# Optimization experiments

Hardware: AMD Instinct MI355X
Metric: run time of the kernel (lower is better)

The kernel has to match this reference:

```python
import jax, jax.numpy as jnp
import numpy as np

# Hardcoded class-anchor table from the original module's target_map ('0'..'9').
_TARGET_MAP = np.array([
    [0, 0.333, 0.333, 0.333, 0.333, 0.333, 0.333, 0.333, 0.333, 0.333],
    [1, 0.0, 0.0, 0.0, 0.0, 0.0, 0.0, 0.0, 0.0, 0.0],
    [0, -0.118, 0.943, -0.118, -0.118, -0.118, -0.118, -0.118, -0.118, -0.118],
    [0, -0.134, 1.78e-16, 0.935, -0.134, -0.134, -0.134, -0.134, -0.134, -0.134],
    [0, -0.154, 1.999e-16, 3.997e-16, 0.926, -0.154, -0.154, -0.154, -0.154, -0.154],
    [0, -0.183, 1.824e-16, 3.953e-16, 6.081e-17, 0.913, -0.183, -0.183, -0.183, -0.183],
    [0, -0.224, 1.738e-16, 4.469e-16, 7.448e-17, -9.93e-17, 0.894, -0.224, -0.224, -0.224],
    [0, -0.289, 2.134e-16, 4.914e-16, 6.41e-17, -1.282e-16, 1.282e-16, 0.866, -0.289, -0.289],
    [0, -0.408, 3.108e-16, 7.576e-16, 9.712e-17, -1.165e-16, 2.331e-16, -3.885e-17, 0.816, -0.408],
    [0, -0.707, 5.103e-16, 1.178e-15, 1.963e-16, -1.57e-16, 3.14e-16, -3.925e-17, -2.355e-16, 0.707],
], dtype=np.float32)

MARGIN_ADV_ANCHOR = 0.5
MARGIN_ADV_MOST_CONFUSING = 0.5
BATCH = 4_000_000
NUM_CLASSES = 10


def setup_inputs() -> dict:
    key = jax.random.key(0)
    k1, k2 = jax.random.split(key)
    x1 = jax.random.normal(k1, (BATCH, NUM_CLASSES), dtype=jnp.float32)
    target = jax.random.randint(k2, (BATCH,), 0, NUM_CLASSES, dtype=jnp.int64 if jax.config.jax_enable_x64 else jnp.int32)
    emb = jnp.asarray(_TARGET_MAP)  # [10, 10] constant class-anchor table
    return {"x1": x1, "target": target, "emb": emb}


def reference(x1, target, emb):
    # Gather per-sample anchor embedding (replaces the per-element python loop).
    x2 = emb[target]                              # [B, 10]
    x1_norm = jnp.sqrt(jnp.sum(x1 * x1, axis=1))  # [B]
    x2_norm = jnp.sqrt(jnp.sum(x2 * x2, axis=1))  # [B]
    adv_anchor_cos = 1.0 - jnp.sum(x1 * x2, axis=1) / (x1_norm * x2_norm)

    # Normalize x1, score against every class anchor in one GEMM.
    x1n = x1 / x1_norm[:, None]                   # [B, 10]
    score = jnp.einsum('bd,cd->bc', x1n, emb)     # [B, 10]

    # Most-confusing class: best-scoring class, or second-best if it equals the label.
    _, top2 = jax.lax.top_k(score, 2)             # [B, 2] int indices
    mc = jnp.where(top2[:, 0] != target, top2[:, 0], top2[:, 1])  # [B]

    x2b = emb[mc]                                 # [B, 10]
    x1n_norm = jnp.sqrt(jnp.sum(x1n * x1n, axis=1))
    x2b_norm = jnp.sqrt(jnp.sum(x2b * x2b, axis=1))
    adv_mc_cos = 1.0 - jnp.sum(x1n * x2b, axis=1) / (x1n_norm * x2b_norm)

    penalty_loss = jnp.maximum(MARGIN_ADV_MOST_CONFUSING - adv_mc_cos, 0.0)
    anchor_loss = jnp.maximum(adv_anchor_cos - MARGIN_ADV_ANCHOR, 0.0)
    return jnp.mean(penalty_loss + anchor_loss)
```

## Files before the change

### kernel.cpp

```cpp
#include <hip/hip_runtime.h>

#define NC 10
#define SPC 512
#define F4PC ((SPC * NC) / 4)
#define NBLOCKS 2048

typedef float f32x4 __attribute__((ext_vector_type(4)));

__device__ __forceinline__ float sample_loss(const float* x, int tg, const float* icn)
{
    float T8 = x[9];
    float T7 = x[8] + T8;
    float T6 = x[7] + T7;
    float T5 = x[6] + T6;
    float T4 = x[5] + T5;
    float T3 = x[4] + T4;
    float T2 = x[3] + T3;
    float T1 = x[2] + T2;
    float S  = x[1] + T1;

    float d[NC];
    d[0] = 0.333f * S;
    d[1] = x[0];
    d[2] = fmaf(0.943f, x[2], -0.118f * (x[1] + T2));
    d[3] = fmaf(0.935f, x[3], -0.134f * (x[1] + T3));
    d[4] = fmaf(0.926f, x[4], -0.154f * (x[1] + T4));
    d[5] = fmaf(0.913f, x[5], -0.183f * (x[1] + T5));
    d[6] = fmaf(0.894f, x[6], -0.224f * (x[1] + T6));
    d[7] = fmaf(0.866f, x[7], -0.289f * (x[1] + T7));
    d[8] = fmaf(0.816f, x[8], -0.408f * (x[1] + T8));
    d[9] = 0.707f * (x[9] - x[1]);

    float self = x[0] * x[0];
#pragma unroll
    for (int i = 1; i < NC; ++i) self = fmaf(x[i], x[i], self);
    float inv1 = __frsqrt_rn(self);

    float best = -3.0e38f, icnb = 1.f, dt = 0.f, icnt = 1.f;
#pragma unroll
    for (int c = 0; c < NC; ++c) {
        bool istg = (c == tg);
        dt   = istg ? d[c]   : dt;
        icnt = istg ? icn[c] : icnt;
        float dc = istg ? -3.0e38f : d[c];
        bool gt = dc > best;
        best = gt ? dc     : best;
        icnb = gt ? icn[c] : icnb;
    }
    float simmc = best * icnb * inv1;
    float simt  = dt   * icnt * inv1;
    return fmaxf(simmc - 0.5f, 0.f) + fmaxf(0.5f - simt, 0.f);
}

__global__ __launch_bounds__(256) void margin_loss_kernel(
    const float* __restrict__ x1,
    const int* __restrict__ target,
    float* __restrict__ partial,
    int B)
{
    __shared__ float lds[SPC * NC];
    __shared__ float swave[4];

    constexpr float N2[NC] = {
        9.f * 0.333f * 0.333f,
        1.f,
        0.943f * 0.943f + 8.f * 0.118f * 0.118f,
        0.935f * 0.935f + 7.f * 0.134f * 0.134f,
        0.926f * 0.926f + 6.f * 0.154f * 0.154f,
        0.913f * 0.913f + 5.f * 0.183f * 0.183f,
        0.894f * 0.894f + 4.f * 0.224f * 0.224f,
        0.866f * 0.866f + 3.f * 0.289f * 0.289f,
        0.816f * 0.816f + 2.f * 0.408f * 0.408f,
        2.f * 0.707f * 0.707f
    };
    float icn[NC];
#pragma unroll
    for (int c = 0; c < NC; ++c) icn[c] = __frsqrt_rn(N2[c]);

    const int tid = threadIdx.x;
    const f32x4* __restrict__ x14 = (const f32x4*)x1;
    f32x4* lds4 = (f32x4*)lds;
    const long maxf4 = (long)B * NC / 4;
    const int nchunks = (B + SPC - 1) / SPC;
    float local = 0.f;

    for (int chunk = blockIdx.x; chunk < nchunks; chunk += (int)gridDim.x) {
        long base = (long)chunk * F4PC;
        if (base + F4PC <= maxf4) {
#pragma unroll
            for (int k = 0; k < 5; ++k)
                lds4[k * 256 + tid] = __builtin_nontemporal_load(&x14[base + k * 256 + tid]);
        } else {
#pragma unroll
            for (int k = 0; k < 5; ++k) {
                long g = base + k * 256 + tid;
                if (g > maxf4 - 1) g = maxf4 - 1;
                lds4[k * 256 + tid] = __builtin_nontemporal_load(&x14[g]);
            }
        }
        __syncthreads();

        int s0 = chunk * SPC + tid * 2;
        const f32x4* vf = (const f32x4*)(lds + tid * 20);
        if (s0 + 1 < B) {
            long long tt = __builtin_nontemporal_load((const long long*)(target + s0));
            int tga = (int)(tt & 0xffffffff);
            int tgb = (int)(tt >> 32);
            f32x4 a0 = vf[0], a1 = vf[1], a2 = vf[2], a3 = vf[3], a4 = vf[4];
            float xa[NC] = {a0.x,a0.y,a0.z,a0.w,a1.x,a1.y,a1.z,a1.w,a2.x,a2.y};
            float xb[NC] = {a2.z,a2.w,a3.x,a3.y,a3.z,a3.w,a4.x,a4.y,a4.z,a4.w};
            local += sample_loss(xa, tga, icn);
            local += sample_loss(xb, tgb, icn);
        } else if (s0 < B) {
            f32x4 a0 = vf[0], a1 = vf[1], a2 = vf[2];
            float xa[NC] = {a0.x,a0.y,a0.z,a0.w,a1.x,a1.y,a1.z,a1.w,a2.x,a2.y};
            local += sample_loss(xa, target[s0], icn);
        }
        __syncthreads();
    }

#pragma unroll
    for (int off = 32; off > 0; off >>= 1) local += __shfl_down(local, off, 64);
    int lane = tid & 63;
    int wid  = tid >> 6;
    if (lane == 0) swave[wid] = local;
    __syncthreads();
    if (tid == 0)
        partial[blockIdx.x] = swave[0] + swave[1] + swave[2] + swave[3];
}

__global__ __launch_bounds__(256) void reduce_kernel(
    const float* __restrict__ partial, float* __restrict__ out, int n, float scale)
{
    float local = 0.f;
    for (int i = threadIdx.x; i < n; i += 256) local += partial[i];
#pragma unroll
    for (int off = 32; off > 0; off >>= 1) local += __shfl_down(local, off, 64);
    __shared__ float swave[4];
    int lane = threadIdx.x & 63;
    int wid  = threadIdx.x >> 6;
    if (lane == 0) swave[wid] = local;
    __syncthreads();
    if (threadIdx.x == 0)
        out[0] = (swave[0] + swave[1] + swave[2] + swave[3]) * scale;
}

extern "C" void kernel_launch(void* const* d_in, const int* in_sizes, int n_in,
                              void* d_out, int out_size, void* d_ws, size_t ws_size,
                              hipStream_t stream) {
    const float* x1     = (const float*)d_in[0];
    const int*   target = (const int*)d_in[1];
    float* out     = (float*)d_out;
    float* partial = (float*)d_ws;
    int B = in_sizes[1];

    margin_loss_kernel<<<NBLOCKS, 256, 0, stream>>>(x1, target, partial, B);
    reduce_kernel<<<1, 256, 0, stream>>>(partial, out, NBLOCKS, 1.0f / (float)B);
}
```

Baseline: 221.3 us.

## Replace LDS-staged chunk loop with register double-buffered direct per-thread loads

Removes the shared-memory staging and the two block barriers per chunk. Each thread now loads its two samples' 80 bytes and targets directly into registers in a grid-stride loop, prefetching the next pair while computing the current one. This is meant to keep more memory requests in flight and avoid barrier stalls. The cost is strided, less coalesced per-instruction access patterns and higher register pressure. An odd trailing sample is handled separately by one thread.

```diff
diff --git a/kernel.cpp b/kernel.cpp
--- a/kernel.cpp
+++ b/kernel.cpp
@@ -1,11 +1,29 @@
 #include <hip/hip_runtime.h>
 
 #define NC 10
-#define SPC 512
-#define F4PC ((SPC * NC) / 4)
 #define NBLOCKS 2048
+#define NTHREADS 256
 
 typedef float f32x4 __attribute__((ext_vector_type(4)));
+
+struct Pair {
+    f32x4 a0, a1, a2, a3, a4;
+    int tga, tgb;
+};
+
+__device__ __forceinline__ void load_pair(Pair& P, const float* __restrict__ x1,
+                                          const int* __restrict__ target, long p)
+{
+    const f32x4* r4 = (const f32x4*)(x1 + p * 2 * NC);
+    P.a0 = __builtin_nontemporal_load(r4 + 0);
+    P.a1 = __builtin_nontemporal_load(r4 + 1);
+    P.a2 = __builtin_nontemporal_load(r4 + 2);
+    P.a3 = __builtin_nontemporal_load(r4 + 3);
+    P.a4 = __builtin_nontemporal_load(r4 + 4);
+    long long tt = __builtin_nontemporal_load((const long long*)(target + 2 * p));
+    P.tga = (int)(tt & 0xffffffff);
+    P.tgb = (int)(tt >> 32);
+}
 
 __device__ __forceinline__ float sample_loss(const float* x, int tg, const float* icn)
 {
@@ -52,15 +70,19 @@
     return fmaxf(simmc - 0.5f, 0.f) + fmaxf(0.5f - simt, 0.f);
 }
 
-__global__ __launch_bounds__(256) void margin_loss_kernel(
+__device__ __forceinline__ float pair_loss(const Pair& P, const float* icn)
+{
+    float xa[NC] = {P.a0.x,P.a0.y,P.a0.z,P.a0.w,P.a1.x,P.a1.y,P.a1.z,P.a1.w,P.a2.x,P.a2.y};
+    float xb[NC] = {P.a2.z,P.a2.w,P.a3.x,P.a3.y,P.a3.z,P.a3.w,P.a4.x,P.a4.y,P.a4.z,P.a4.w};
+    return sample_loss(xa, P.tga, icn) + sample_loss(xb, P.tgb, icn);
+}
+
+__global__ __launch_bounds__(NTHREADS, 4) void margin_loss_kernel(
     const float* __restrict__ x1,
     const int* __restrict__ target,
     float* __restrict__ partial,
     int B)
 {
-    __shared__ float lds[SPC * NC];
-    __shared__ float swave[4];
-
     constexpr float N2[NC] = {
         9.f * 0.333f * 0.333f,
         1.f,
@@ -77,55 +99,38 @@
 #pragma unroll
     for (int c = 0; c < NC; ++c) icn[c] = __frsqrt_rn(N2[c]);
 
-    const int tid = threadIdx.x;
-    const f32x4* __restrict__ x14 = (const f32x4*)x1;
-    f32x4* lds4 = (f32x4*)lds;
-    const long maxf4 = (long)B * NC / 4;
-    const int nchunks = (B + SPC - 1) / SPC;
+    const long npairs = (long)(B >> 1);
+    const long stride = (long)gridDim.x * blockDim.x;
+    long p = (long)blockIdx.x * blockDim.x + threadIdx.x;
+
     float local = 0.f;
-
-    for (int chunk = blockIdx.x; chunk < nchunks; chunk += (int)gridDim.x) {
-        long base = (long)chunk * F4PC;
-        if (base + F4PC <= maxf4) {
+    Pair cur, nxt;
+    bool have = p < npairs;
+    if (have) load_pair(cur, x1, target, p);
+    while (have) {
+        long pn = p + stride;
+        bool haven = pn < npairs;
+        if (haven) load_pair(nxt, x1, target, pn);
+        local += pair_loss(cur, icn);
+        cur = nxt;
+        p = pn;
+        have = haven;
+    }
+    if ((B & 1) && blockIdx.x == 0 && threadIdx.x == 0) {
+        float xa[NC];
 #pragma unroll
-            for (int k = 0; k < 5; ++k)
-                lds4[k * 256 + tid] = __builtin_nontemporal_load(&x14[base + k * 256 + tid]);
-        } else {
-#pragma unroll
-            for (int k = 0; k < 5; ++k) {
-                long g = base + k * 256 + tid;
-                if (g > maxf4 - 1) g = maxf4 - 1;
-                lds4[k * 256 + tid] = __builtin_nontemporal_load(&x14[g]);
-            }
-        }
-        __syncthreads();
-
-        int s0 = chunk * SPC + tid * 2;
-        const f32x4* vf = (const f32x4*)(lds + tid * 20);
-        if (s0 + 1 < B) {
-            long long tt = __builtin_nontemporal_load((const long long*)(target + s0));
-            int tga = (int)(tt & 0xffffffff);
-            int tgb = (int)(tt >> 32);
-            f32x4 a0 = vf[0], a1 = vf[1], a2 = vf[2], a3 = vf[3], a4 = vf[4];
-            float xa[NC] = {a0.x,a0.y,a0.z,a0.w,a1.x,a1.y,a1.z,a1.w,a2.x,a2.y};
-            float xb[NC] = {a2.z,a2.w,a3.x,a3.y,a3.z,a3.w,a4.x,a4.y,a4.z,a4.w};
-            local += sample_loss(xa, tga, icn);
-            local += sample_loss(xb, tgb, icn);
-        } else if (s0 < B) {
-            f32x4 a0 = vf[0], a1 = vf[1], a2 = vf[2];
-            float xa[NC] = {a0.x,a0.y,a0.z,a0.w,a1.x,a1.y,a1.z,a1.w,a2.x,a2.y};
-            local += sample_loss(xa, target[s0], icn);
-        }
-        __syncthreads();
+        for (int i = 0; i < NC; ++i) xa[i] = x1[(long)(B - 1) * NC + i];
+        local += sample_loss(xa, target[B - 1], icn);
     }
 
 #pragma unroll
     for (int off = 32; off > 0; off >>= 1) local += __shfl_down(local, off, 64);
-    int lane = tid & 63;
-    int wid  = tid >> 6;
+    __shared__ float swave[NTHREADS / 64];
+    int lane = threadIdx.x & 63;
+    int wid  = threadIdx.x >> 6;
     if (lane == 0) swave[wid] = local;
     __syncthreads();
-    if (tid == 0)
+    if (threadIdx.x == 0)
         partial[blockIdx.x] = swave[0] + swave[1] + swave[2] + swave[3];
 }
 
@@ -154,6 +159,6 @@
     float* partial = (float*)d_ws;
     int B = in_sizes[1];
 
-    margin_loss_kernel<<<NBLOCKS, 256, 0, stream>>>(x1, target, partial, B);
+    margin_loss_kernel<<<NBLOCKS, NTHREADS, 0, stream>>>(x1, target, partial, B);
     reduce_kernel<<<1, 256, 0, stream>>>(partial, out, NBLOCKS, 1.0f / (float)B);
 }
```

Measured after the change: 247.1 us. 1.12x slower.

## Use direct global-to-LDS loads with one chunk per block grid

Applied to the files above, without the earlier changes.

Replaces the grid-stride loop over 2048 blocks with one block per 512-sample chunk (about 7800 blocks). It loads x1 into LDS with global_load_lds (buffer-to-LDS DMA) instead of round-tripping through registers, and issues the target load before the tile load. It also hardcodes the inverse anchor norms and widens the final reduction to 1024 threads to handle the larger partial array. The intent is to remove VGPR staging and per-iteration barriers and expose more memory parallelism, at the cost of more block launches and a bigger second-stage reduction.

```diff
diff --git a/kernel.cpp b/kernel.cpp
--- a/kernel.cpp
+++ b/kernel.cpp
@@ -3,12 +3,20 @@
 #define NC 10
 #define SPC 512
 #define F4PC ((SPC * NC) / 4)
-#define NBLOCKS 2048
+#define NTHREADS 256
 
 typedef float f32x4 __attribute__((ext_vector_type(4)));
+typedef const __attribute__((address_space(1))) void* gas_ptr;
+typedef __attribute__((address_space(3))) void* las_ptr;
+typedef __attribute__((address_space(3))) f32x4* las_f4;
 
-__device__ __forceinline__ float sample_loss(const float* x, int tg, const float* icn)
+__device__ __forceinline__ float sample_loss(const float* x, int tg)
 {
+    constexpr float icn[NC] = {
+        1.00100100f, 1.00000000f, 0.99967966f, 1.00004150f, 1.00011402f,
+        0.99949338f, 1.00003000f, 0.99974060f, 1.00060855f, 1.00015103f
+    };
+
     float T8 = x[9];
     float T7 = x[8] + T8;
     float T6 = x[7] + T7;
@@ -52,71 +60,63 @@
     return fmaxf(simmc - 0.5f, 0.f) + fmaxf(0.5f - simt, 0.f);
 }
 
-__global__ __launch_bounds__(256) void margin_loss_kernel(
+__global__ __launch_bounds__(NTHREADS) void margin_loss_kernel(
     const float* __restrict__ x1,
     const int* __restrict__ target,
     float* __restrict__ partial,
     int B)
 {
     __shared__ float lds[SPC * NC];
-    __shared__ float swave[4];
+    __shared__ float swave[NTHREADS / 64];
 
-    constexpr float N2[NC] = {
-        9.f * 0.333f * 0.333f,
-        1.f,
-        0.943f * 0.943f + 8.f * 0.118f * 0.118f,
-        0.935f * 0.935f + 7.f * 0.134f * 0.134f,
-        0.926f * 0.926f + 6.f * 0.154f * 0.154f,
-        0.913f * 0.913f + 5.f * 0.183f * 0.183f,
-        0.894f * 0.894f + 4.f * 0.224f * 0.224f,
-        0.866f * 0.866f + 3.f * 0.289f * 0.289f,
-        0.816f * 0.816f + 2.f * 0.408f * 0.408f,
-        2.f * 0.707f * 0.707f
-    };
-    float icn[NC];
+    const int tid   = threadIdx.x;
+    const int chunk = blockIdx.x;
+    const long maxf4 = (long)B * NC / 4;
+    const long base  = (long)chunk * F4PC;
+    const f32x4* __restrict__ x14 = (const f32x4*)x1;
+
+    int s0 = chunk * SPC + tid * 2;
+    bool full = (s0 + 1 < B);
+    int tga = 0, tgb = 0;
+    if (full) {
+        long long tt = __builtin_nontemporal_load((const long long*)(target + s0));
+        tga = (int)(tt & 0xffffffff);
+        tgb = (int)(tt >> 32);
+    } else if (s0 < B) {
+        tga = target[s0];
+    }
+
+    const int wbase = tid & ~63;
+    las_f4 ldsa = (las_f4)lds;
+    if (base + F4PC <= maxf4) {
 #pragma unroll
-    for (int c = 0; c < NC; ++c) icn[c] = __frsqrt_rn(N2[c]);
+        for (int k = 0; k < 5; ++k)
+            __builtin_amdgcn_global_load_lds((gas_ptr)(x14 + base + k * 256 + tid),
+                                             (las_ptr)(ldsa + k * 256 + wbase),
+                                             16, 0, 0);
+    } else {
+#pragma unroll
+        for (int k = 0; k < 5; ++k) {
+            long g = base + k * 256 + tid;
+            if (g > maxf4 - 1) g = maxf4 - 1;
+            __builtin_amdgcn_global_load_lds((gas_ptr)(x14 + g),
+                                             (las_ptr)(ldsa + k * 256 + wbase),
+                                             16, 0, 0);
+        }
+    }
+    __syncthreads();
 
-    const int tid = threadIdx.x;
-    const f32x4* __restrict__ x14 = (const f32x4*)x1;
-    f32x4* lds4 = (f32x4*)lds;
-    const long maxf4 = (long)B * NC / 4;
-    const int nchunks = (B + SPC - 1) / SPC;
     float local = 0.f;
-
-    for (int chunk = blockIdx.x; chunk < nchunks; chunk += (int)gridDim.x) {
-        long base = (long)chunk * F4PC;
-        if (base + F4PC <= maxf4) {
-#pragma unroll
-            for (int k = 0; k < 5; ++k)
-                lds4[k * 256 + tid] = __builtin_nontemporal_load(&x14[base + k * 256 + tid]);
-        } else {
-#pragma unroll
-            for (int k = 0; k < 5; ++k) {
-                long g = base + k * 256 + tid;
-                if (g > maxf4 - 1) g = maxf4 - 1;
-                lds4[k * 256 + tid] = __builtin_nontemporal_load(&x14[g]);
-            }
-        }
-        __syncthreads();
-
-        int s0 = chunk * SPC + tid * 2;
-        const f32x4* vf = (const f32x4*)(lds + tid * 20);
-        if (s0 + 1 < B) {
-            long long tt = __builtin_nontemporal_load((const long long*)(target + s0));
-            int tga = (int)(tt & 0xffffffff);
-            int tgb = (int)(tt >> 32);
-            f32x4 a0 = vf[0], a1 = vf[1], a2 = vf[2], a3 = vf[3], a4 = vf[4];
-            float xa[NC] = {a0.x,a0.y,a0.z,a0.w,a1.x,a1.y,a1.z,a1.w,a2.x,a2.y};
-            float xb[NC] = {a2.z,a2.w,a3.x,a3.y,a3.z,a3.w,a4.x,a4.y,a4.z,a4.w};
-            local += sample_loss(xa, tga, icn);
-            local += sample_loss(xb, tgb, icn);
-        } else if (s0 < B) {
-            f32x4 a0 = vf[0], a1 = vf[1], a2 = vf[2];
-            float xa[NC] = {a0.x,a0.y,a0.z,a0.w,a1.x,a1.y,a1.z,a1.w,a2.x,a2.y};
-            local += sample_loss(xa, target[s0], icn);
-        }
-        __syncthreads();
+    const f32x4* vf = (const f32x4*)(lds + tid * 20);
+    if (full) {
+        f32x4 a0 = vf[0], a1 = vf[1], a2 = vf[2], a3 = vf[3], a4 = vf[4];
+        float xa[NC] = {a0.x,a0.y,a0.z,a0.w,a1.x,a1.y,a1.z,a1.w,a2.x,a2.y};
+        float xb[NC] = {a2.z,a2.w,a3.x,a3.y,a3.z,a3.w,a4.x,a4.y,a4.z,a4.w};
+        local = sample_loss(xa, tga) + sample_loss(xb, tgb);
+    } else if (s0 < B) {
+        f32x4 a0 = vf[0], a1 = vf[1], a2 = vf[2];
+        float xa[NC] = {a0.x,a0.y,a0.z,a0.w,a1.x,a1.y,a1.z,a1.w,a2.x,a2.y};
+        local = sample_loss(xa, tga);
     }
 
 #pragma unroll
@@ -129,20 +129,24 @@
         partial[blockIdx.x] = swave[0] + swave[1] + swave[2] + swave[3];
 }
 
-__global__ __launch_bounds__(256) void reduce_kernel(
+__global__ __launch_bounds__(1024) void reduce_kernel(
     const float* __restrict__ partial, float* __restrict__ out, int n, float scale)
 {
     float local = 0.f;
-    for (int i = threadIdx.x; i < n; i += 256) local += partial[i];
+    for (int i = threadIdx.x; i < n; i += 1024) local += partial[i];
 #pragma unroll
     for (int off = 32; off > 0; off >>= 1) local += __shfl_down(local, off, 64);
-    __shared__ float swave[4];
+    __shared__ float swave[16];
     int lane = threadIdx.x & 63;
     int wid  = threadIdx.x >> 6;
     if (lane == 0) swave[wid] = local;
     __syncthreads();
-    if (threadIdx.x == 0)
-        out[0] = (swave[0] + swave[1] + swave[2] + swave[3]) * scale;
+    if (threadIdx.x == 0) {
+        float s = 0.f;
+#pragma unroll
+        for (int i = 0; i < 16; ++i) s += swave[i];
+        out[0] = s * scale;
+    }
 }
 
 extern "C" void kernel_launch(void* const* d_in, const int* in_sizes, int n_in,
@@ -154,6 +158,7 @@
     float* partial = (float*)d_ws;
     int B = in_sizes[1];
 
-    margin_loss_kernel<<<NBLOCKS, 256, 0, stream>>>(x1, target, partial, B);
-    reduce_kernel<<<1, 256, 0, stream>>>(partial, out, NBLOCKS, 1.0f / (float)B);
+    int nchunks = (B + SPC - 1) / SPC;
+    margin_loss_kernel<<<nchunks, NTHREADS, 0, stream>>>(x1, target, partial, B);
+    reduce_kernel<<<1, 1024, 0, stream>>>(partial, out, nchunks, 1.0f / (float)B);
 }
```

Result: slower. 231.5 us (+4.6%).
